# Optimization experiments

Measured on AMD Instinct MI355X. Metric: run time of the kernel, lower is better.

The kernel has to match this reference:

```python
import jax, jax.numpy as jnp
import numpy as np

B, S, D = 2, 2048, 1024
H, DK, DV = 16, 64, 64
MASKED = True


def setup_inputs() -> dict:
    key = jax.random.key(0)
    ks = jax.random.split(key, 12)
    s = 0.02
    inp = {
        "Q": jax.random.normal(ks[0], (B, S, D), jnp.float32),
        "K": jax.random.normal(ks[1], (B, S, D), jnp.float32),
        "V": jax.random.normal(ks[2], (B, S, D), jnp.float32),
        "pad_mask": jax.random.randint(ks[3], (B, S), 0, 2, jnp.int32),
        "Wq": jax.random.normal(ks[4], (D, H * DK), jnp.float32) * s,
        "bq": jnp.zeros((H * DK,), jnp.float32),
        "Wk": jax.random.normal(ks[5], (D, H * DK), jnp.float32) * s,
        "bk": jnp.zeros((H * DK,), jnp.float32),
        "Wv": jax.random.normal(ks[6], (D, H * DV), jnp.float32) * s,
        "bv": jnp.zeros((H * DV,), jnp.float32),
        "Wo": jax.random.normal(ks[7], (H * DV, D), jnp.float32) * s,
        "bo": jnp.zeros((D,), jnp.float32),
    }
    return inp


def _split(x):
    # [B,S,H*d] -> [B,H,S,d]
    b, s, _ = x.shape
    return x.reshape(b, s, H, -1).transpose(0, 2, 1, 3)


def reference(Q, K, V, pad_mask, Wq, bq, Wk, bk, Wv, bv, Wo, bo):
    q = _split(Q @ Wq + bq)  # [B,H,S,DK]
    k = _split(K @ Wk + bk)  # [B,H,S,DK]
    v = _split(V @ Wv + bv)  # [B,H,S,DV]

    scores = jnp.einsum("bhqd,bhkd->bhqk", q, k) / np.sqrt(DK)
    mask = pad_mask[:, None, None, :].astype(jnp.float32)  # [B,1,1,S]
    if MASKED:
        causal = jnp.triu(jnp.ones((S, S), jnp.float32), k=1)[None, None]
        mask = ((mask + causal) > 0).astype(jnp.float32)
    scores = scores - 1e9 * mask

    attn = jax.nn.softmax(scores, axis=-1)
    out = jnp.einsum("bhqk,bhkd->bhqd", attn, v)  # [B,H,S,DV]
    out = out.transpose(0, 2, 1, 3).reshape(B, S, H * DV)
    return out @ Wo + bo
```

## Files before the change

### kernel.cpp

```cpp
#include <hip/hip_runtime.h>

typedef unsigned short u16;
typedef unsigned int u32;

typedef __attribute__((ext_vector_type(8))) short bfrag;
typedef __attribute__((ext_vector_type(4))) float f32x4;
typedef __attribute__((ext_vector_type(8))) u16 u16x8;
typedef __attribute__((ext_vector_type(4))) u16 u16x4;

constexpr int S = 2048;
constexpr int HN = 16;
constexpr float QSCALE = 0.18033688011112042f;
constexpr float NBIG   = -1.442695e9f;

__device__ __forceinline__ u16 f2b(float f) {
  u32 u = __builtin_bit_cast(u32, f);
  return (u16)((u + 0x7FFFu + ((u >> 16) & 1u)) >> 16);
}
__device__ __forceinline__ float b2f(u16 v) {
  u32 u = (u32)v << 16;
  return __builtin_bit_cast(float, u);
}
__device__ __forceinline__ u32 cvtpk(float lo, float hi) {
  u32 d;
  asm("v_cvt_pk_bf16_f32 %0, %1, %2" : "=v"(d) : "v"(lo), "v"(hi));
  return d;
}
__device__ __forceinline__ float fexp2(float x) { return __builtin_amdgcn_exp2f(x); }

__device__ __forceinline__ f32x4 mfma16(bfrag a, bfrag b, f32x4 c) {
  return __builtin_amdgcn_mfma_f32_16x16x32_bf16(a, b, c, 0, 0, 0);
}

__device__ __forceinline__ void gload_lds16(const void* g, void* l) {
  __builtin_amdgcn_global_load_lds(
      (const __attribute__((address_space(1))) u32*)g,
      (__attribute__((address_space(3))) u32*)l, 16, 0, 0);
}

__global__ __launch_bounds__(256) void wtrans_kernel(
    const float* __restrict__ W0, const float* __restrict__ W1,
    const float* __restrict__ W2, const float* __restrict__ W3,
    u16* __restrict__ ws)
{
  const float* W = blockIdx.z == 0 ? W0 : blockIdx.z == 1 ? W1 : blockIdx.z == 2 ? W2 : W3;
  const float sc = blockIdx.z == 0 ? QSCALE : 1.0f;
  u16* WT = ws + (size_t)blockIdx.z * (1u << 20);
  __shared__ u16 tile[64 * 65];
  const int t = threadIdx.x;
  const int k0 = blockIdx.y * 64, n0 = blockIdx.x * 64;
#pragma unroll
  for (int i = 0; i < 4; ++i) {
    int idx = i * 256 + t;
    int r = idx >> 4, c4 = (idx & 15) * 4;
    float4 v = *(const float4*)&W[(size_t)(k0 + r) * 1024 + n0 + c4];
    tile[r * 65 + c4 + 0] = f2b(v.x * sc);
    tile[r * 65 + c4 + 1] = f2b(v.y * sc);
    tile[r * 65 + c4 + 2] = f2b(v.z * sc);
    tile[r * 65 + c4 + 3] = f2b(v.w * sc);
  }
  __syncthreads();
#pragma unroll
  for (int i = 0; i < 2; ++i) {
    int idx = i * 256 + t;
    int n = idx >> 3, k8 = (idx & 7) * 8;
    u16x8 o;
#pragma unroll
    for (int j = 0; j < 8; ++j) o[j] = tile[(k8 + j) * 65 + n];
    *(u16x8*)&WT[(size_t)(n0 + n) * 1024 + k0 + k8] = o;
  }
}

__global__ __launch_bounds__(256) void cvt_kernel(
    const float* __restrict__ A0, const float* __restrict__ A1,
    const float* __restrict__ A2, u16* __restrict__ outbase)
{
  const float* A = blockIdx.y == 0 ? A0 : blockIdx.y == 1 ? A1 : A2;
  u16* dst = outbase + (size_t)blockIdx.y * (4u << 20);
  size_t i = ((size_t)blockIdx.x * 256 + threadIdx.x) * 8;
  float4 v0 = *(const float4*)&A[i];
  float4 v1 = *(const float4*)&A[i + 4];
  union { u32 w[4]; u16x8 v; } o;
  o.w[0] = cvtpk(v0.x, v0.y); o.w[1] = cvtpk(v0.z, v0.w);
  o.w[2] = cvtpk(v1.x, v1.y); o.w[3] = cvtpk(v1.z, v1.w);
  *(u16x8*)&dst[i] = o.v;
}

__global__ __launch_bounds__(256) void pscan_kernel(
    const int* __restrict__ pad, u16* __restrict__ idxc, int* __restrict__ eqt,
    float* __restrict__ colsumg)
{
  __shared__ int wtot[4];
  __shared__ int cntS;
  const int b = blockIdx.x;
  const int t = threadIdx.x, lane = t & 63, w = t >> 6;
  for (int i = t; i < 1024; i += 256) colsumg[b * 1024 + i] = 0.f;
  int4 p0 = *(const int4*)&pad[b * 2048 + t * 8];
  int4 p1 = *(const int4*)&pad[b * 2048 + t * 8 + 4];
  int u[8] = {p0.x == 0, p0.y == 0, p0.z == 0, p0.w == 0,
              p1.x == 0, p1.y == 0, p1.z == 0, p1.w == 0};
  int ps[8], run = 0;
#pragma unroll
  for (int j = 0; j < 8; ++j) { run += u[j]; ps[j] = run; }
  int sc = run;
#pragma unroll
  for (int o = 1; o < 64; o <<= 1) {
    int v = __shfl_up(sc, o);
    if (lane >= o) sc += v;
  }
  if (lane == 63) wtot[w] = sc;
  __syncthreads();
  int base = 0;
#pragma unroll
  for (int i = 0; i < 4; ++i) if (i < w) base += wtot[i];
  int excl = base + sc - run;
#pragma unroll
  for (int j = 0; j < 8; ++j)
    if (u[j]) idxc[b * 2048 + excl + ps[j] - 1] = (u16)(t * 8 + j);
  if ((t & 7) == 7) eqt[b * 32 + (t >> 3)] = base + sc;
  if (t == 255) cntS = base + sc;
  __syncthreads();
  for (int j = cntS + t; j < 2048; j += 256) idxc[b * 2048 + j] = 0x7FFF;
}

__global__ __launch_bounds__(256) void colsum_kernel(
    const u16* __restrict__ v, float* __restrict__ colsumg)
{
  const int bh = blockIdx.x >> 3, seg = blockIdx.x & 7;
  const int t = threadIdx.x;
  const int c8 = t & 7, rq = t >> 3;
  float acc[8] = {};
  for (int it = 0; it < 8; ++it) {
    int row = seg * 256 + it * 32 + rq;
    u16x8 x = *(const u16x8*)&v[((size_t)bh * 2048 + row) * 64 + c8 * 8];
#pragma unroll
    for (int j = 0; j < 8; ++j) acc[j] += b2f(x[j]);
  }
#pragma unroll
  for (int o = 8; o < 64; o <<= 1)
#pragma unroll
    for (int j = 0; j < 8; ++j) acc[j] += __shfl_xor(acc[j], o);
  if ((t & 63) < 8) {
#pragma unroll
    for (int j = 0; j < 8; ++j)
      atomicAdd(&colsumg[bh * 64 + c8 * 8 + j], acc[j]);
  }
}

__global__ __launch_bounds__(256) void kvgather_kernel(
    const u16* __restrict__ kb, const u16* __restrict__ vb,
    const u16* __restrict__ idxc, u16* __restrict__ kc, u16* __restrict__ vTc)
{
  __shared__ u16 tile[64 * 65];
  const int ti = blockIdx.x, bh = blockIdx.y, b = bh >> 4;
  const int t = threadIdx.x;

#pragma unroll
  for (int pass = 0; pass < 2; ++pass) {
    int jl = pass * 32 + (t >> 3), db = t & 7;
    int j = ti * 64 + jl;
    int o = idxc[b * 2048 + j];
    u16x8 val = {};
    if (o != 0x7FFF)
      val = *(const u16x8*)&kb[((size_t)bh * 2048 + o) * 64 + db * 8];
    *(u16x8*)&kc[((size_t)bh * 2048 + j) * 64 + (db ^ (j & 7)) * 8] = val;
  }

#pragma unroll
  for (int i = 0; i < 2; ++i) {
    int idx = i * 256 + t;
    int r = idx >> 3, c8 = (idx & 7) * 8;
    int o = idxc[b * 2048 + ti * 64 + r];
    u16x8 in = {};
    if (o != 0x7FFF) in = *(const u16x8*)&vb[((size_t)bh * 2048 + o) * 64 + c8];
#pragma unroll
    for (int j = 0; j < 8; ++j) tile[r * 65 + c8 + j] = in[j];
  }
  __syncthreads();
#pragma unroll
  for (int i = 0; i < 2; ++i) {
    int idx = i * 256 + t;
    int dv = idx >> 3, s8 = (idx & 7) * 8;
    u16x8 o_;
#pragma unroll
    for (int j = 0; j < 8; ++j) o_[j] = tile[(s8 + j) * 65 + dv];
    int a = s8 >> 5, bb = (s8 >> 4) & 1, cc = (s8 >> 3) & 1;
    int s0l = a * 32 + cc * 16 + bb * 4;
    int x = (dv & 7) << 3;
    u16x4 lo = {o_[0], o_[1], o_[2], o_[3]};
    u16x4 hi = {o_[4], o_[5], o_[6], o_[7]};
    size_t rowbase = ((size_t)bh * 64 + dv) * S + ti * 64;
    *(u16x4*)&vTc[rowbase + (s0l ^ x)] = lo;
    *(u16x4*)&vTc[rowbase + ((s0l + 8) ^ x)] = hi;
  }
}

template <int AMODE, int CMODE>
__device__ __forceinline__ void gemm_core(
    u16* As, u16* Bs,
    const void* __restrict__ Av, const u16* __restrict__ Bt,
    const float* __restrict__ bias, void* __restrict__ Cout,
    int N, int K, int bn, int bm, float bscale)
{
  const int tid = threadIdx.x;
  const int wid = tid >> 6, lane = tid & 63;
  const int g = lane >> 4, c = lane & 15;
  const int wr = wid >> 1, wc = wid & 1;

  f32x4 acc[4][2] = {};

  const int nkt = K >> 6;
  for (int kt = 0; kt < nkt; ++kt) {
    if (AMODE == 0) {
      const float* A = (const float*)Av;
#pragma unroll
      for (int p = 0; p < 4; ++p) {
        int e = (p * 256 + tid) * 8;
        int row = e >> 6, col = e & 63;
        const float* src = &A[(size_t)(bm * 128 + row) * K + kt * 64 + col];
        float4 v0 = *(const float4*)src;
        float4 v1 = *(const float4*)(src + 4);
        u16x8 w;
        w[0] = f2b(v0.x); w[1] = f2b(v0.y); w[2] = f2b(v0.z); w[3] = f2b(v0.w);
        w[4] = f2b(v1.x); w[5] = f2b(v1.y); w[6] = f2b(v1.z); w[7] = f2b(v1.w);
        *(u16x8*)&As[row * 64 + (col ^ ((row & 7) << 3))] = w;
      }
    } else {
      const u16* A = (const u16*)Av;
#pragma unroll
      for (int p = 0; p < 4; ++p) {
        int off = (p * 4 + wid) * 1024 + (lane << 4);
        int row = off >> 7, colb = off & 127;
        gload_lds16(&A[(size_t)(bm * 128 + row) * K + kt * 64 +
                       ((colb ^ ((row & 7) << 4)) >> 1)],
                    (char*)As + (p * 4 + wid) * 1024);
      }
    }
#pragma unroll
    for (int p = 0; p < 2; ++p) {
      int off = (p * 4 + wid) * 1024 + (lane << 4);
      int row = off >> 7, colb = off & 127;
      gload_lds16(&Bt[(size_t)(bn * 64 + row) * K + kt * 64 +
                      ((colb ^ ((row & 7) << 4)) >> 1)],
                  (char*)Bs + (p * 4 + wid) * 1024);
    }
    __syncthreads();

#pragma unroll
    for (int ks = 0; ks < 2; ++ks) {
      bfrag af[4], bf[2];
#pragma unroll
      for (int mi = 0; mi < 4; ++mi) {
        int row = wr * 64 + mi * 16 + c;
        af[mi] = *(const bfrag*)&As[row * 64 + ((ks * 32 + g * 8) ^ ((row & 7) << 3))];
      }
#pragma unroll
      for (int ni = 0; ni < 2; ++ni) {
        int row = wc * 32 + ni * 16 + c;
        bf[ni] = *(const bfrag*)&Bs[row * 64 + ((ks * 32 + g * 8) ^ ((row & 7) << 3))];
      }
#pragma unroll
      for (int mi = 0; mi < 4; ++mi)
#pragma unroll
        for (int ni = 0; ni < 2; ++ni)
          acc[mi][ni] = mfma16(af[mi], bf[ni], acc[mi][ni]);
    }
    __syncthreads();
  }

#pragma unroll
  for (int mi = 0; mi < 4; ++mi) {
#pragma unroll
    for (int ni = 0; ni < 2; ++ni) {
#pragma unroll
      for (int j = 0; j < 4; ++j) {
        int rowg = bm * 128 + wr * 64 + mi * 16 + g * 4 + j;
        int colg = bn * 64 + wc * 32 + ni * 16 + c;
        float val = fmaf(bias[colg], bscale, acc[mi][ni][j]);
        if (CMODE == 0) {
          int b = rowg >> 11, s = rowg & (S - 1);
          int h = colg >> 6, d = colg & 63;
          ((u16*)Cout)[((size_t)((b * HN + h) * S + s)) * 64 + d] = f2b(val);
        } else {
          ((float*)Cout)[(size_t)rowg * N + colg] = val;
        }
      }
    }
  }
}

__global__ __launch_bounds__(256) void qkv_gemm_b16(
    const u16* __restrict__ Abase, const u16* __restrict__ WTbase,
    const float* __restrict__ b0, const float* __restrict__ b1, const float* __restrict__ b2,
    u16* __restrict__ wsbase)
{
  __shared__ __align__(16) u16 As[128 * 64];
  __shared__ __align__(16) u16 Bs[64 * 64];
  const int bid = blockIdx.x;
  const int l = (bid & 7) * 192 + (bid >> 3);
  const int z = l >> 9, rem = l & 511, bm = rem >> 4, bn = rem & 15;
  const u16* A = Abase + (size_t)z * (4u << 20);
  const u16* Bt = WTbase + (size_t)z * (1u << 20);
  const float* bias = z == 0 ? b0 : z == 1 ? b1 : b2;
  u16* C = wsbase + (size_t)(4 + 4 * z) * (1u << 20);
  gemm_core<2, 0>(As, Bs, A, Bt, bias, C, 1024, 1024, bn, bm,
                  z == 0 ? QSCALE : 1.0f);
}

__global__ __launch_bounds__(256) void qkv_gemm_f32(
    const float* __restrict__ A0, const float* __restrict__ A1, const float* __restrict__ A2,
    const u16* __restrict__ WTbase,
    const float* __restrict__ b0, const float* __restrict__ b1, const float* __restrict__ b2,
    u16* __restrict__ wsbase)
{
  __shared__ __align__(16) u16 As[128 * 64];
  __shared__ __align__(16) u16 Bs[64 * 64];
  const int z = blockIdx.z;
  const float* A = z == 0 ? A0 : z == 1 ? A1 : A2;
  const u16* Bt = WTbase + (size_t)z * (1u << 20);
  const float* bias = z == 0 ? b0 : z == 1 ? b1 : b2;
  u16* C = wsbase + (size_t)(4 + 4 * z) * (1u << 20);
  gemm_core<0, 0>(As, Bs, A, Bt, bias, C, 1024, 1024, blockIdx.x, blockIdx.y,
                  z == 0 ? QSCALE : 1.0f);
}

__global__ __launch_bounds__(256) void out_gemm(
    const u16* __restrict__ Av, const u16* __restrict__ Bt,
    const float* __restrict__ bias, void* __restrict__ Cout)
{
  __shared__ __align__(16) u16 As[128 * 64];
  __shared__ __align__(16) u16 Bs[64 * 64];
  const int bid = blockIdx.x;
  const int l = (bid & 7) * 64 + (bid >> 3);
  const int bm = l >> 4, bn = l & 15;
  gemm_core<2, 1>(As, Bs, Av, Bt, bias, Cout, 1024, 1024, bn, bm, 1.0f);
}

__global__ __launch_bounds__(256) void attn_kernel(
    const u16* __restrict__ q, const u16* __restrict__ kc,
    const u16* __restrict__ vTc, const u16* __restrict__ idxc,
    const int* __restrict__ eqt, const float* __restrict__ colsumg,
    u16* __restrict__ ao)
{
  __shared__ __align__(16) u16 Ks[2][64 * 64];
  __shared__ __align__(16) u16 Vs[2][64 * 64];

  const int tid = threadIdx.x;
  const int wid = tid >> 6, lane = tid & 63;
  const int g = lane >> 4, c = lane & 15;
  const int i = blockIdx.x;
  const int qt = 31 - (i >> 5);
  const int bh = i & 31;
  const int b = bh >> 4, h = bh & 15;

  const u16* idxb = idxc + b * 2048;
  const int ecnt = eqt[b * 32 + qt];
  const int nt = (ecnt + 63) >> 6;
  const int fz = idxb[0];
  const int qbasew = qt * 64 + wid * 16;
  const int qrow = qbasew + c;

  bfrag qf[2];
#pragma unroll
  for (int ks = 0; ks < 2; ++ks)
    qf[ks] = *(const bfrag*)&q[((size_t)bh * S + qrow) * 64 + ks * 32 + g * 8];

  float m = -3.0e38f, lsum = 0.f;
  f32x4 acc[4] = {};

  const size_t kbase = (size_t)bh * S * 64;
  const size_t vbase = (size_t)bh * 64 * S;
  const int sb = wid * 2048 + (lane << 4);
  const int sb2 = sb + 1024;

#define STAGE(buf, t)                                                              \
  do {                                                                             \
    gload_lds16(&kc[kbase + (size_t)(t) * 4096 + (sb >> 1)],                       \
                (char*)Ks[buf] + wid * 2048);                                      \
    gload_lds16(&kc[kbase + (size_t)(t) * 4096 + (sb2 >> 1)],                      \
                (char*)Ks[buf] + wid * 2048 + 1024);                               \
    gload_lds16(&vTc[vbase + (size_t)(sb >> 7) * S + (t) * 64 + ((sb & 127) >> 1)],\
                (char*)Vs[buf] + wid * 2048);                                      \
    gload_lds16(&vTc[vbase + (size_t)(sb2 >> 7) * S + (t) * 64 + ((sb2 & 127) >> 1)],\
                (char*)Vs[buf] + wid * 2048 + 1024);                               \
  } while (0)

  if (nt > 0) {
    STAGE(0, 0);
    __syncthreads();

    int cur = 0;
    for (int t = 0; t < nt; ++t) {
      if (t + 1 < nt) { STAGE(cur ^ 1, t + 1); }

      f32x4 sc[4] = {};
      __builtin_amdgcn_s_setprio(1);
#pragma unroll
      for (int ks = 0; ks < 2; ++ks)
#pragma unroll
        for (int nf = 0; nf < 4; ++nf) {
          int row = nf * 16 + c;
          bfrag kf = *(const bfrag*)&Ks[cur][row * 64 + ((ks * 32 + g * 8) ^ ((row & 7) << 3))];
          sc[nf] = mfma16(kf, qf[ks], sc[nf]);
        }
      __builtin_amdgcn_s_setprio(0);

      float sval[4][4];
#pragma unroll
      for (int nf = 0; nf < 4; ++nf)
#pragma unroll
        for (int r = 0; r < 4; ++r) sval[nf][r] = sc[nf][r];

      if ((int)idxb[t * 64 + 63] > qbasew) {
#pragma unroll
        for (int nf = 0; nf < 4; ++nf)
#pragma unroll
          for (int r = 0; r < 4; ++r) {
            int ov = idxb[t * 64 + nf * 16 + g * 4 + r];
            if (ov > qrow) sval[nf][r] = NBIG;
          }
      }

      float pm = sval[0][0];
#pragma unroll
      for (int nf = 0; nf < 4; ++nf)
#pragma unroll
        for (int r = 0; r < 4; ++r) pm = fmaxf(pm, sval[nf][r]);
      pm = fmaxf(pm, __shfl_xor(pm, 16));
      pm = fmaxf(pm, __shfl_xor(pm, 32));
      if (!__all(pm - m <= 11.5416f)) {
        float mn = fmaxf(m, pm);
        float fac = fexp2(m - mn);
        lsum *= fac;
#pragma unroll
        for (int nf = 0; nf < 4; ++nf)
#pragma unroll
          for (int j = 0; j < 4; ++j) acc[nf][j] *= fac;
        m = mn;
      }
      float p16v[4][4];
      float rs = 0.f;
#pragma unroll
      for (int nf = 0; nf < 4; ++nf)
#pragma unroll
        for (int r = 0; r < 4; ++r) {
          float pv = fexp2(sval[nf][r] - m);
          p16v[nf][r] = pv;
          rs += pv;
        }
      rs += __shfl_xor(rs, 16);
      rs += __shfl_xor(rs, 32);
      lsum += rs;

      bfrag pa[2];
#pragma unroll
      for (int ks = 0; ks < 2; ++ks) {
        union { u32 w[4]; bfrag f; } pu;
#pragma unroll
        for (int tt = 0; tt < 4; ++tt)
          pu.w[tt] = cvtpk(p16v[2 * ks + (tt >> 1)][2 * (tt & 1)],
                           p16v[2 * ks + (tt >> 1)][2 * (tt & 1) + 1]);
        pa[ks] = pu.f;
      }

      __builtin_amdgcn_s_setprio(1);
#pragma unroll
      for (int ks = 0; ks < 2; ++ks)
#pragma unroll
        for (int nf = 0; nf < 4; ++nf) {
          int row = nf * 16 + c;
          bfrag vf = *(const bfrag*)&Vs[cur][row * 64 + ((ks * 32 + g * 8) ^ ((row & 7) << 3))];
          acc[nf] = mfma16(vf, pa[ks], acc[nf]);
        }
      __builtin_amdgcn_s_setprio(0);

      __syncthreads();
      cur ^= 1;
    }
  }
#undef STAGE

  const float inv = 1.f / lsum;
#pragma unroll
  for (int nf = 0; nf < 4; ++nf) {
    u16x4 ov;
    if (qrow < fz) {
#pragma unroll
      for (int j = 0; j < 4; ++j)
        ov[j] = f2b(colsumg[bh * 64 + nf * 16 + g * 4 + j] * (1.f / 2048.f));
    } else {
#pragma unroll
      for (int j = 0; j < 4; ++j) ov[j] = f2b(acc[nf][j] * inv);
    }
    *(u16x4*)&ao[((size_t)b * S + qrow) * 1024 + h * 64 + nf * 16 + g * 4] = ov;
  }
}

extern "C" void kernel_launch(void* const* d_in, const int* in_sizes, int n_in,
                              void* d_out, int out_size, void* d_ws, size_t ws_size,
                              hipStream_t stream)
{
  const float* Q  = (const float*)d_in[0];
  const float* Kk = (const float*)d_in[1];
  const float* V  = (const float*)d_in[2];
  const int* pad  = (const int*)d_in[3];
  const float* Wq = (const float*)d_in[4];
  const float* bq = (const float*)d_in[5];
  const float* Wk = (const float*)d_in[6];
  const float* bk = (const float*)d_in[7];
  const float* Wv = (const float*)d_in[8];
  const float* bv = (const float*)d_in[9];
  const float* Wo = (const float*)d_in[10];
  const float* bo = (const float*)d_in[11];

  u16* ws  = (u16*)d_ws;
  u16* WoT = ws + 3 * (size_t)(1u << 20);
  u16* qb  = ws + 4 * (size_t)(1u << 20);
  u16* kb  = ws + 8 * (size_t)(1u << 20);
  u16* vb  = ws + 12 * (size_t)(1u << 20);
  u16* Abf = ws + 20 * (size_t)(1u << 20);
  u16* kc  = ws + 20 * (size_t)(1u << 20);
  u16* vTc = ws + 24 * (size_t)(1u << 20);
  u16* ao  = vb;
  float* colsumg = (float*)(ws + (1u << 20));
  u16* idxc = ws + (1u << 20) + 4096;
  int* eqt  = (int*)(ws + (1u << 20) + 8192);

  const bool big = ws_size >= (size_t)64 * 1024 * 1024;

  wtrans_kernel<<<dim3(16, 16, 4), 256, 0, stream>>>(Wq, Wk, Wv, Wo, ws);
  if (big) {
    cvt_kernel<<<dim3(2048, 3), 256, 0, stream>>>(Q, Kk, V, Abf);
    qkv_gemm_b16<<<1536, 256, 0, stream>>>(Abf, ws, bq, bk, bv, ws);
  } else {
    qkv_gemm_f32<<<dim3(16, 32, 3), 256, 0, stream>>>(Q, Kk, V, ws, bq, bk, bv, ws);
  }
  pscan_kernel<<<2, 256, 0, stream>>>(pad, idxc, eqt, colsumg);
  colsum_kernel<<<256, 256, 0, stream>>>(vb, colsumg);
  kvgather_kernel<<<dim3(32, 32), 256, 0, stream>>>(kb, vb, idxc, kc, vTc);
  attn_kernel<<<1024, 256, 0, stream>>>(qb, kc, vTc, idxc, eqt, colsumg, ao);
  out_gemm<<<512, 256, 0, stream>>>(ao, WoT, bo, d_out);
}
```

Baseline: 116.7 us.

## Fuse fp32-to-bf16 conversion and K compaction into QKV GEMM

Removes the separate cvt_kernel by DMA-loading fp32 activations straight into LDS, using a swizzled layout, and converting to bf16 when fragments are read. It also drops the K gather pass: pscan now emits an inverse permutation (posT), and the QKV GEMM epilogue scatters K rows directly into their compacted, swizzled positions. This cuts a full bf16 round trip of Q/K/V plus the K gather traffic, at the cost of double the LDS for the A tile, conversion work repeated across N-tiles, and scattered epilogue stores.

```diff
diff --git a/kernel.cpp b/kernel.cpp
--- a/kernel.cpp
+++ b/kernel.cpp
@@ -71,24 +71,9 @@
   }
 }
 
-__global__ __launch_bounds__(256) void cvt_kernel(
-    const float* __restrict__ A0, const float* __restrict__ A1,
-    const float* __restrict__ A2, u16* __restrict__ outbase)
-{
-  const float* A = blockIdx.y == 0 ? A0 : blockIdx.y == 1 ? A1 : A2;
-  u16* dst = outbase + (size_t)blockIdx.y * (4u << 20);
-  size_t i = ((size_t)blockIdx.x * 256 + threadIdx.x) * 8;
-  float4 v0 = *(const float4*)&A[i];
-  float4 v1 = *(const float4*)&A[i + 4];
-  union { u32 w[4]; u16x8 v; } o;
-  o.w[0] = cvtpk(v0.x, v0.y); o.w[1] = cvtpk(v0.z, v0.w);
-  o.w[2] = cvtpk(v1.x, v1.y); o.w[3] = cvtpk(v1.z, v1.w);
-  *(u16x8*)&dst[i] = o.v;
-}
-
 __global__ __launch_bounds__(256) void pscan_kernel(
-    const int* __restrict__ pad, u16* __restrict__ idxc, int* __restrict__ eqt,
-    float* __restrict__ colsumg)
+    const int* __restrict__ pad, u16* __restrict__ idxc, u16* __restrict__ posT,
+    int* __restrict__ eqt, float* __restrict__ colsumg)
 {
   __shared__ int wtot[4];
   __shared__ int cntS;
@@ -120,7 +105,14 @@
   if ((t & 7) == 7) eqt[b * 32 + (t >> 3)] = base + sc;
   if (t == 255) cntS = base + sc;
   __syncthreads();
-  for (int j = cntS + t; j < 2048; j += 256) idxc[b * 2048 + j] = 0x7FFF;
+  const int cnt = cntS;
+#pragma unroll
+  for (int j = 0; j < 8; ++j) {
+    int e = t * 8 + j;
+    int pv = u[j] ? (excl + ps[j] - 1) : (cnt + e - excl - ps[j]);
+    posT[b * 2048 + e] = (u16)pv;
+  }
+  for (int j = cnt + t; j < 2048; j += 256) idxc[b * 2048 + j] = 0x7FFF;
 }
 
 __global__ __launch_bounds__(256) void colsum_kernel(
@@ -147,25 +139,12 @@
   }
 }
 
-__global__ __launch_bounds__(256) void kvgather_kernel(
-    const u16* __restrict__ kb, const u16* __restrict__ vb,
-    const u16* __restrict__ idxc, u16* __restrict__ kc, u16* __restrict__ vTc)
+__global__ __launch_bounds__(256) void vgather_kernel(
+    const u16* __restrict__ vb, const u16* __restrict__ idxc, u16* __restrict__ vTc)
 {
   __shared__ u16 tile[64 * 65];
   const int ti = blockIdx.x, bh = blockIdx.y, b = bh >> 4;
   const int t = threadIdx.x;
-
-#pragma unroll
-  for (int pass = 0; pass < 2; ++pass) {
-    int jl = pass * 32 + (t >> 3), db = t & 7;
-    int j = ti * 64 + jl;
-    int o = idxc[b * 2048 + j];
-    u16x8 val = {};
-    if (o != 0x7FFF)
-      val = *(const u16x8*)&kb[((size_t)bh * 2048 + o) * 64 + db * 8];
-    *(u16x8*)&kc[((size_t)bh * 2048 + j) * 64 + (db ^ (j & 7)) * 8] = val;
-  }
-
 #pragma unroll
   for (int i = 0; i < 2; ++i) {
     int idx = i * 256 + t;
@@ -200,7 +179,7 @@
     u16* As, u16* Bs,
     const void* __restrict__ Av, const u16* __restrict__ Bt,
     const float* __restrict__ bias, void* __restrict__ Cout,
-    int N, int K, int bn, int bm, float bscale)
+    int N, int K, int bn, int bm, float bscale, const u16* __restrict__ posT)
 {
   const int tid = threadIdx.x;
   const int wid = tid >> 6, lane = tid & 63;
@@ -211,21 +190,7 @@
 
   const int nkt = K >> 6;
   for (int kt = 0; kt < nkt; ++kt) {
-    if (AMODE == 0) {
-      const float* A = (const float*)Av;
-#pragma unroll
-      for (int p = 0; p < 4; ++p) {
-        int e = (p * 256 + tid) * 8;
-        int row = e >> 6, col = e & 63;
-        const float* src = &A[(size_t)(bm * 128 + row) * K + kt * 64 + col];
-        float4 v0 = *(const float4*)src;
-        float4 v1 = *(const float4*)(src + 4);
-        u16x8 w;
-        w[0] = f2b(v0.x); w[1] = f2b(v0.y); w[2] = f2b(v0.z); w[3] = f2b(v0.w);
-        w[4] = f2b(v1.x); w[5] = f2b(v1.y); w[6] = f2b(v1.z); w[7] = f2b(v1.w);
-        *(u16x8*)&As[row * 64 + (col ^ ((row & 7) << 3))] = w;
-      }
-    } else {
+    if (AMODE == 2) {
       const u16* A = (const u16*)Av;
 #pragma unroll
       for (int p = 0; p < 4; ++p) {
@@ -233,6 +198,17 @@
         int row = off >> 7, colb = off & 127;
         gload_lds16(&A[(size_t)(bm * 128 + row) * K + kt * 64 +
                        ((colb ^ ((row & 7) << 4)) >> 1)],
+                    (char*)As + (p * 4 + wid) * 1024);
+      }
+    } else {
+      const float* A = (const float*)Av;
+#pragma unroll
+      for (int p = 0; p < 8; ++p) {
+        int off = (p * 4 + wid) * 1024 + (lane << 4);
+        int row = off >> 8;
+        int grp = (off >> 4) & 15;
+        gload_lds16(&A[(size_t)(bm * 128 + row) * K + kt * 64 +
+                       ((grp ^ (row & 15)) << 2)],
                     (char*)As + (p * 4 + wid) * 1024);
       }
     }
@@ -252,7 +228,18 @@
 #pragma unroll
       for (int mi = 0; mi < 4; ++mi) {
         int row = wr * 64 + mi * 16 + c;
-        af[mi] = *(const bfrag*)&As[row * 64 + ((ks * 32 + g * 8) ^ ((row & 7) << 3))];
+        if (AMODE == 2) {
+          af[mi] = *(const bfrag*)&As[row * 64 + ((ks * 32 + g * 8) ^ ((row & 7) << 3))];
+        } else {
+          const char* rb = (const char*)As + row * 256;
+          int g0 = ks * 8 + g * 2;
+          float4 lo = *(const float4*)(rb + ((g0 ^ (row & 15)) << 4));
+          float4 hi = *(const float4*)(rb + (((g0 + 1) ^ (row & 15)) << 4));
+          union { u32 w[4]; bfrag f; } cu;
+          cu.w[0] = cvtpk(lo.x, lo.y); cu.w[1] = cvtpk(lo.z, lo.w);
+          cu.w[2] = cvtpk(hi.x, hi.y); cu.w[3] = cvtpk(hi.z, hi.w);
+          af[mi] = cu.f;
+        }
       }
 #pragma unroll
       for (int ni = 0; ni < 2; ++ni) {
@@ -280,6 +267,11 @@
         if (CMODE == 0) {
           int b = rowg >> 11, s = rowg & (S - 1);
           int h = colg >> 6, d = colg & 63;
+          if (posT) {
+            int p_ = posT[(b << 11) | s];
+            s = p_;
+            d = (d & 7) | ((((d >> 3) ^ p_) & 7) << 3);
+          }
           ((u16*)Cout)[((size_t)((b * HN + h) * S + s)) * 64 + d] = f2b(val);
         } else {
           ((float*)Cout)[(size_t)rowg * N + colg] = val;
@@ -289,39 +281,24 @@
   }
 }
 
-__global__ __launch_bounds__(256) void qkv_gemm_b16(
-    const u16* __restrict__ Abase, const u16* __restrict__ WTbase,
+__global__ __launch_bounds__(256) void qkv_gemm(
+    const float* __restrict__ Q, const float* __restrict__ Kk, const float* __restrict__ V,
+    const u16* __restrict__ WTbase,
     const float* __restrict__ b0, const float* __restrict__ b1, const float* __restrict__ b2,
-    u16* __restrict__ wsbase)
-{
-  __shared__ __align__(16) u16 As[128 * 64];
+    u16* __restrict__ qb, u16* __restrict__ kc, u16* __restrict__ vb,
+    const u16* __restrict__ posT)
+{
+  __shared__ __align__(16) u16 As[128 * 128];
   __shared__ __align__(16) u16 Bs[64 * 64];
   const int bid = blockIdx.x;
   const int l = (bid & 7) * 192 + (bid >> 3);
   const int z = l >> 9, rem = l & 511, bm = rem >> 4, bn = rem & 15;
-  const u16* A = Abase + (size_t)z * (4u << 20);
+  const float* A = z == 0 ? Q : z == 1 ? Kk : V;
   const u16* Bt = WTbase + (size_t)z * (1u << 20);
   const float* bias = z == 0 ? b0 : z == 1 ? b1 : b2;
-  u16* C = wsbase + (size_t)(4 + 4 * z) * (1u << 20);
-  gemm_core<2, 0>(As, Bs, A, Bt, bias, C, 1024, 1024, bn, bm,
-                  z == 0 ? QSCALE : 1.0f);
-}
-
-__global__ __launch_bounds__(256) void qkv_gemm_f32(
-    const float* __restrict__ A0, const float* __restrict__ A1, const float* __restrict__ A2,
-    const u16* __restrict__ WTbase,
-    const float* __restrict__ b0, const float* __restrict__ b1, const float* __restrict__ b2,
-    u16* __restrict__ wsbase)
-{
-  __shared__ __align__(16) u16 As[128 * 64];
-  __shared__ __align__(16) u16 Bs[64 * 64];
-  const int z = blockIdx.z;
-  const float* A = z == 0 ? A0 : z == 1 ? A1 : A2;
-  const u16* Bt = WTbase + (size_t)z * (1u << 20);
-  const float* bias = z == 0 ? b0 : z == 1 ? b1 : b2;
-  u16* C = wsbase + (size_t)(4 + 4 * z) * (1u << 20);
-  gemm_core<0, 0>(As, Bs, A, Bt, bias, C, 1024, 1024, blockIdx.x, blockIdx.y,
-                  z == 0 ? QSCALE : 1.0f);
+  u16* C = z == 0 ? qb : z == 1 ? kc : vb;
+  gemm_core<3, 0>(As, Bs, A, Bt, bias, C, 1024, 1024, bn, bm,
+                  z == 0 ? QSCALE : 1.0f, z == 1 ? posT : nullptr);
 }
 
 __global__ __launch_bounds__(256) void out_gemm(
@@ -333,7 +310,7 @@
   const int bid = blockIdx.x;
   const int l = (bid & 7) * 64 + (bid >> 3);
   const int bm = l >> 4, bn = l & 15;
-  gemm_core<2, 1>(As, Bs, Av, Bt, bias, Cout, 1024, 1024, bn, bm, 1.0f);
+  gemm_core<2, 1>(As, Bs, Av, Bt, bias, Cout, 1024, 1024, bn, bm, 1.0f, nullptr);
 }
 
 __global__ __launch_bounds__(256) void attn_kernel(
@@ -516,28 +493,21 @@
   u16* ws  = (u16*)d_ws;
   u16* WoT = ws + 3 * (size_t)(1u << 20);
   u16* qb  = ws + 4 * (size_t)(1u << 20);
-  u16* kb  = ws + 8 * (size_t)(1u << 20);
+  u16* kc  = ws + 8 * (size_t)(1u << 20);
   u16* vb  = ws + 12 * (size_t)(1u << 20);
-  u16* Abf = ws + 20 * (size_t)(1u << 20);
-  u16* kc  = ws + 20 * (size_t)(1u << 20);
-  u16* vTc = ws + 24 * (size_t)(1u << 20);
-  u16* ao  = vb;
-  float* colsumg = (float*)(ws + (1u << 20));
-  u16* idxc = ws + (1u << 20) + 4096;
-  int* eqt  = (int*)(ws + (1u << 20) + 8192);
-
-  const bool big = ws_size >= (size_t)64 * 1024 * 1024;
+  u16* vTc = ws + 16 * (size_t)(1u << 20);
+  u16* tab = ws + 20 * (size_t)(1u << 20);
+  float* colsumg = (float*)tab;
+  u16* idxc = tab + 4096;
+  u16* posT = tab + 8192;
+  int* eqt  = (int*)(tab + 12288);
+  u16* ao   = vb;
 
   wtrans_kernel<<<dim3(16, 16, 4), 256, 0, stream>>>(Wq, Wk, Wv, Wo, ws);
-  if (big) {
-    cvt_kernel<<<dim3(2048, 3), 256, 0, stream>>>(Q, Kk, V, Abf);
-    qkv_gemm_b16<<<1536, 256, 0, stream>>>(Abf, ws, bq, bk, bv, ws);
-  } else {
-    qkv_gemm_f32<<<dim3(16, 32, 3), 256, 0, stream>>>(Q, Kk, V, ws, bq, bk, bv, ws);
-  }
-  pscan_kernel<<<2, 256, 0, stream>>>(pad, idxc, eqt, colsumg);
+  pscan_kernel<<<2, 256, 0, stream>>>(pad, idxc, posT, eqt, colsumg);
+  qkv_gemm<<<1536, 256, 0, stream>>>(Q, Kk, V, ws, bq, bk, bv, qb, kc, vb, posT);
   colsum_kernel<<<256, 256, 0, stream>>>(vb, colsumg);
-  kvgather_kernel<<<dim3(32, 32), 256, 0, stream>>>(kb, vb, idxc, kc, vTc);
+  vgather_kernel<<<dim3(32, 32), 256, 0, stream>>>(vb, idxc, vTc);
   attn_kernel<<<1024, 256, 0, stream>>>(qb, kc, vTc, idxc, eqt, colsumg, ao);
   out_gemm<<<512, 256, 0, stream>>>(ao, WoT, bo, d_out);
 }
```

New measurement: 125.7 us. +7.7%, slower.
